# Kernel optimization log

Measured on AMD Instinct MI355X. Metric: run time of the kernel, lower is better.

Reference implementation:

```python
import jax, jax.numpy as jnp
import numpy as np

N, E = 50000, 800000
IN_DIM, E_DIM, OUT_DIM, H = 128, 32, 16, 4
NEG_SLOPE = 0.2


def setup_inputs() -> dict:
    key = jax.random.key(0)
    ks = jax.random.split(key, 9)
    return {
        "feat": jax.random.normal(ks[0], (N, IN_DIM), jnp.float32),
        "edge_attr": jax.random.normal(ks[1], (E, E_DIM), jnp.float32),
        "src": jax.random.randint(ks[2], (E,), 0, N),
        "dst": jax.random.randint(ks[3], (E,), 0, N),
        "W_fc": jax.random.normal(ks[4], (OUT_DIM * H, IN_DIM), jnp.float32) * 0.1,
        "W_edge": jax.random.normal(ks[5], (OUT_DIM * H, E_DIM), jnp.float32) * 0.1,
        "attn_h": jax.random.normal(ks[6], (1, H, OUT_DIM), jnp.float32) * 0.1,
        "attn_t": jax.random.normal(ks[7], (1, H, OUT_DIM), jnp.float32) * 0.1,
        "attn_e": jax.random.normal(ks[8], (1, H, OUT_DIM), jnp.float32) * 0.1,
        "bias": jnp.zeros((1, H, OUT_DIM), jnp.float32),
    }


def reference(feat, edge_attr, src, dst, W_fc, W_edge, attn_h, attn_t, attn_e, bias):
    n = feat.shape[0]
    # node / edge projections
    feat_ = (feat @ W_fc.T).reshape(n, H, OUT_DIM)          # [N,H,D]
    eh = (feat_ * attn_h).sum(-1)                            # [N,H]
    et = (feat_ * attn_t).sum(-1)                            # [N,H]
    feat_e = (edge_attr @ W_edge.T).reshape(-1, H, OUT_DIM)  # [E,H,D]
    ee = (feat_e * attn_e).sum(-1)                           # [E,H]
    # per-edge attention logits: u_add_e then e_add_v, then leaky relu
    e = eh[src] + ee + et[dst]                               # [E,H]
    e = jnp.where(e > 0, e, NEG_SLOPE * e)
    # edge softmax grouped by destination node
    e_max = jax.ops.segment_max(e, dst, num_segments=n)      # [N,H]
    e_max = jnp.where(jnp.isfinite(e_max), e_max, 0.0)
    a = jnp.exp(e - e_max[dst])                              # [E,H]
    a_sum = jax.ops.segment_sum(a, dst, num_segments=n)      # [N,H]
    a = a / jnp.where(a_sum[dst] > 0, a_sum[dst], 1.0)
    # u_mul_e + sum aggregation
    msg = feat_[src] * a[:, :, None]                         # [E,H,D]
    rst = jax.ops.segment_sum(msg, dst, num_segments=n)      # [N,H,D]
    rst = rst + bias
    return rst.reshape(n, H * OUT_DIM)                       # concat_out
```

## Files before the change

### kernel.cpp

```cpp
#include <hip/hip_runtime.h>

#define NN 50000
#define EE 800000
#define IND 128
#define EDD 32
#define ODD 16
#define NH 4
#define HD 64
#define NEG_SLOPE 0.2f
#define NBLK ((NN + 255) / 256)

__global__ __launch_bounds__(256)
void k_init_prep(int* __restrict__ deg, const float* __restrict__ W_fc,
                 const float* __restrict__ W_edge, const float* __restrict__ attn_e,
                 float* __restrict__ Wt, float* __restrict__ w_ee) {
    int i = blockIdx.x * 256 + threadIdx.x;
    if (i < NN) deg[i] = 0;
    if (i < HD * IND) {
        int k = i >> 6, j = i & 63;
        Wt[i] = W_fc[j * IND + k];
    }
    if (i < NH * EDD) {
        int h = i >> 5, k = i & 31;
        float s = 0.f;
        for (int d = 0; d < ODD; ++d)
            s += W_edge[(h * ODD + d) * EDD + k] * attn_e[h * ODD + d];
        w_ee[i] = s;
    }
}

__global__ __launch_bounds__(256)
void k_node(const float* __restrict__ feat, const float* __restrict__ Wt,
            const float* __restrict__ attn_h, const float* __restrict__ attn_t,
            float* __restrict__ feat_ws, float2* __restrict__ eh2,
            float2* __restrict__ et2) {
    int n = blockIdx.x * 256 + threadIdx.x;
    int half = blockIdx.y;
    if (n >= NN) return;
    const int jbase = half * 32;
    float4 row[32];
    const float4* fr4 = (const float4*)(feat + (long)n * IND);
#pragma unroll
    for (int q = 0; q < 32; ++q) row[q] = fr4[q];
    asm volatile("" ::: "memory");
    float acc[32];
#pragma unroll
    for (int j = 0; j < 32; ++j) acc[j] = 0.f;
#pragma unroll
    for (int k0 = 0; k0 < 32; ++k0) {
        float f[4] = {row[k0].x, row[k0].y, row[k0].z, row[k0].w};
#pragma unroll
        for (int kk = 0; kk < 4; ++kk) {
            const float* w = Wt + (k0 * 4 + kk) * HD + jbase;
#pragma unroll
            for (int j = 0; j < 32; ++j) acc[j] += f[kk] * w[j];
        }
    }
    float4* d4 = (float4*)(feat_ws + (long)n * HD + jbase);
#pragma unroll
    for (int q = 0; q < 8; ++q)
        d4[q] = make_float4(acc[q*4], acc[q*4+1], acc[q*4+2], acc[q*4+3]);
    float sh[2], st[2];
#pragma unroll
    for (int hh = 0; hh < 2; ++hh) {
        sh[hh] = 0.f; st[hh] = 0.f;
        int hg = half * 2 + hh;
#pragma unroll
        for (int d = 0; d < ODD; ++d) {
            float av = acc[hh * ODD + d];
            sh[hh] += av * attn_h[hg * ODD + d];
            st[hh] += av * attn_t[hg * ODD + d];
        }
    }
    eh2[n * 2 + half] = make_float2(sh[0], sh[1]);
    et2[n * 2 + half] = make_float2(st[0], st[1]);
}

__global__ __launch_bounds__(256)
void k_hist(const int* __restrict__ dst, int* __restrict__ deg, int* __restrict__ rank) {
    int e = blockIdx.x * 256 + threadIdx.x;
    if (e < EE) rank[e] = atomicAdd(&deg[dst[e]], 1);
}

__global__ __launch_bounds__(256)
void k_scan1(const int* __restrict__ deg, int* __restrict__ offs, int* __restrict__ part) {
    __shared__ int s[256];
    int t = threadIdx.x, i = blockIdx.x * 256 + t;
    int v = (i < NN) ? deg[i] : 0;
    s[t] = v;
    __syncthreads();
#pragma unroll
    for (int o = 1; o < 256; o <<= 1) {
        int u = (t >= o) ? s[t - o] : 0;
        __syncthreads();
        if (t >= o) s[t] += u;
        __syncthreads();
    }
    if (i < NN) offs[i] = s[t] - v;
    if (t == 255) part[blockIdx.x] = s[255];
}

__global__ __launch_bounds__(256)
void k_scan2(int* __restrict__ part) {
    __shared__ int s[256];
    int t = threadIdx.x;
    int v = (t < NBLK) ? part[t] : 0;
    s[t] = v;
    __syncthreads();
#pragma unroll
    for (int o = 1; o < 256; o <<= 1) {
        int u = (t >= o) ? s[t - o] : 0;
        __syncthreads();
        if (t >= o) s[t] += u;
        __syncthreads();
    }
    if (t < NBLK) part[t] = s[t] - v;
}

__global__ __launch_bounds__(256)
void k_scan3(int* __restrict__ offs, const int* __restrict__ part) {
    int i = blockIdx.x * 256 + threadIdx.x;
    if (i < NN) offs[i] += part[i >> 8];
}

__global__ __launch_bounds__(256)
void k_logit2(const float* __restrict__ edge_attr, const int* __restrict__ dst,
              const float* __restrict__ w_ee, const int* __restrict__ offs,
              const int* __restrict__ rank, float4* __restrict__ ee4,
              int* __restrict__ perm) {
    int t = blockIdx.x * 256 + threadIdx.x;
    int e0 = t * 2;
    if (e0 >= EE) return;
    int2 d2 = *(const int2*)(dst + e0);
    int2 r2 = *(const int2*)(rank + e0);
    int   o0 = offs[d2.x], o1 = offs[d2.y];
    const float4* ea = (const float4*)(edge_attr + (long)e0 * EDD);
    float4 r[16];
#pragma unroll
    for (int c = 0; c < 16; ++c) r[c] = ea[c];
    asm volatile("" ::: "memory");
    const float* f0 = (const float*)&r[0];
    const float* f1 = (const float*)&r[8];
    float x0[NH], x1[NH];
#pragma unroll
    for (int h = 0; h < NH; ++h) {
        float a = 0.f, b = 0.f;
#pragma unroll
        for (int k = 0; k < EDD; ++k) {
            float w = w_ee[h * EDD + k];
            a += f0[k] * w;
            b += f1[k] * w;
        }
        x0[h] = a; x1[h] = b;
    }
    ee4[e0]     = make_float4(x0[0], x0[1], x0[2], x0[3]);
    ee4[e0 + 1] = make_float4(x1[0], x1[1], x1[2], x1[3]);
    perm[o0 + r2.x] = e0;
    perm[o1 + r2.y] = e0 + 1;
}

__global__ __launch_bounds__(256)
void k_reduce(const int* __restrict__ offs, const int* __restrict__ deg,
              const float* __restrict__ ee, const float* __restrict__ eh,
              const float* __restrict__ et, const int* __restrict__ perm,
              const int* __restrict__ src, const float* __restrict__ feat_ws,
              const float* __restrict__ bias, float* __restrict__ out) {
    int wid = (blockIdx.x * 256 + threadIdx.x) >> 6;
    int lane = threadIdx.x & 63;
    if (wid >= NN) return;
    int start = __builtin_amdgcn_readfirstlane(offs[wid]);
    int dn    = __builtin_amdgcn_readfirstlane(deg[wid]);
    int h = lane >> 4;
    int q = lane & 15;
    float et_h = et[(long)wid * 4 + h];
    float acc = 0.f, l = 0.f;

    for (int c0 = 0; c0 < dn; c0 += 16) {
        int rem = dn - c0; if (rem > 16) rem = 16;
        int qq = (q < rem) ? q : (rem - 1);
        int   e_q = perm[start + c0 + qq];
        int   s_q = src[e_q];
        float ee_q = ee[(long)e_q * 4 + h];
        float eh_q = eh[(long)s_q * 4 + h];
        float x = ee_q + eh_q + et_h;
        x = x > 0.f ? x : NEG_SLOPE * x;
        float a_q = (q < rem) ? __expf(x) : 0.f;
        float f[16];
#pragma unroll
        for (int i = 0; i < 16; ++i) {
            int si = __shfl(s_q, i);
            f[i] = feat_ws[(long)si * HD + lane];
        }
#pragma unroll
        for (int i = 0; i < 16; ++i) {
            float ai = __shfl(a_q, (lane & 48) + i);
            l += ai;
            acc += ai * f[i];
        }
    }
    float res = (l > 0.f) ? acc / l : 0.f;
    out[(long)wid * HD + lane] = res + bias[lane];
}

extern "C" void kernel_launch(void* const* d_in, const int* in_sizes, int n_in,
                              void* d_out, int out_size, void* d_ws, size_t ws_size,
                              hipStream_t stream) {
    const float* feat      = (const float*)d_in[0];
    const float* edge_attr = (const float*)d_in[1];
    const int*   src       = (const int*)d_in[2];
    const int*   dst       = (const int*)d_in[3];
    const float* W_fc      = (const float*)d_in[4];
    const float* W_edge    = (const float*)d_in[5];
    const float* attn_h    = (const float*)d_in[6];
    const float* attn_t    = (const float*)d_in[7];
    const float* attn_e    = (const float*)d_in[8];
    const float* bias      = (const float*)d_in[9];
    float* out             = (float*)d_out;

    float* ws        = (float*)d_ws;
    float4* ee4      = (float4*)ws;
    float4* eh4      = ee4 + EE;
    float4* et4      = eh4 + NN;
    float*  feat_ws  = (float*)(et4 + NN);
    float*  Wt       = feat_ws + (long)NN * HD;
    float*  w_ee     = Wt + HD * IND;
    int*    perm     = (int*)(w_ee + NH * EDD);
    int*    rank     = perm + EE;
    int*    deg      = rank + EE;
    int*    offs     = deg + NN;
    int*    part     = offs + NN;

    k_init_prep<<<NBLK, 256, 0, stream>>>(deg, W_fc, W_edge, attn_e, Wt, w_ee);
    dim3 ngrid(NBLK, 2);
    k_node<<<ngrid, 256, 0, stream>>>(feat, Wt, attn_h, attn_t, feat_ws,
                                      (float2*)eh4, (float2*)et4);
    k_hist<<<(EE + 255) / 256, 256, 0, stream>>>(dst, deg, rank);
    k_scan1<<<NBLK, 256, 0, stream>>>(deg, offs, part);
    k_scan2<<<1, 256, 0, stream>>>(part);
    k_scan3<<<NBLK, 256, 0, stream>>>(offs, part);
    k_logit2<<<(EE / 2 + 255) / 256, 256, 0, stream>>>(edge_attr, dst, w_ee, offs, rank,
                                                       ee4, perm);
    k_reduce<<<(NN * 64 + 255) / 256, 256, 0, stream>>>(offs, deg, (const float*)ee4,
                                                        (const float*)eh4, (const float*)et4,
                                                        perm, src, feat_ws, bias, out);
}
```

Measured before the change: 336.3 us.

## Fuse edge logit+exp into sorted-order edge pass, store node features in fp16

New measurement: 383.4 us. +14.0%, slower.

```diff
diff --git a/kernel.cpp b/kernel.cpp
--- a/kernel.cpp
+++ b/kernel.cpp
@@ -10,6 +10,10 @@
 #define NEG_SLOPE 0.2f
 #define NBLK ((NN + 255) / 256)
 
+typedef float  f32x4 __attribute__((ext_vector_type(4)));
+typedef int    i32x2 __attribute__((ext_vector_type(2)));
+typedef _Float16 f16x8 __attribute__((ext_vector_type(8)));
+
 __global__ __launch_bounds__(256)
 void k_init_prep(int* __restrict__ deg, const float* __restrict__ W_fc,
                  const float* __restrict__ W_edge, const float* __restrict__ attn_e,
@@ -32,23 +36,23 @@
 __global__ __launch_bounds__(256)
 void k_node(const float* __restrict__ feat, const float* __restrict__ Wt,
             const float* __restrict__ attn_h, const float* __restrict__ attn_t,
-            float* __restrict__ feat_ws, float2* __restrict__ eh2,
+            _Float16* __restrict__ feat_h, float2* __restrict__ eh2,
             float2* __restrict__ et2) {
     int n = blockIdx.x * 256 + threadIdx.x;
-    int half = blockIdx.y;
+    int hf = blockIdx.y;
     if (n >= NN) return;
-    const int jbase = half * 32;
-    float4 row[32];
-    const float4* fr4 = (const float4*)(feat + (long)n * IND);
-#pragma unroll
-    for (int q = 0; q < 32; ++q) row[q] = fr4[q];
+    const int jbase = hf * 32;
+    f32x4 row[32];
+    const f32x4* fr4 = (const f32x4*)(feat + (long)n * IND);
+#pragma unroll
+    for (int q = 0; q < 32; ++q) row[q] = __builtin_nontemporal_load(fr4 + q);
     asm volatile("" ::: "memory");
     float acc[32];
 #pragma unroll
     for (int j = 0; j < 32; ++j) acc[j] = 0.f;
 #pragma unroll
     for (int k0 = 0; k0 < 32; ++k0) {
-        float f[4] = {row[k0].x, row[k0].y, row[k0].z, row[k0].w};
+        float f[4] = {row[k0][0], row[k0][1], row[k0][2], row[k0][3]};
 #pragma unroll
         for (int kk = 0; kk < 4; ++kk) {
             const float* w = Wt + (k0 * 4 + kk) * HD + jbase;
@@ -56,15 +60,19 @@
             for (int j = 0; j < 32; ++j) acc[j] += f[kk] * w[j];
         }
     }
-    float4* d4 = (float4*)(feat_ws + (long)n * HD + jbase);
-#pragma unroll
-    for (int q = 0; q < 8; ++q)
-        d4[q] = make_float4(acc[q*4], acc[q*4+1], acc[q*4+2], acc[q*4+3]);
+    f16x8* d8 = (f16x8*)(feat_h + (long)n * HD + jbase);
+#pragma unroll
+    for (int q = 0; q < 4; ++q) {
+        f16x8 v;
+#pragma unroll
+        for (int j = 0; j < 8; ++j) v[j] = (_Float16)acc[q * 8 + j];
+        d8[q] = v;
+    }
     float sh[2], st[2];
 #pragma unroll
     for (int hh = 0; hh < 2; ++hh) {
         sh[hh] = 0.f; st[hh] = 0.f;
-        int hg = half * 2 + hh;
+        int hg = hf * 2 + hh;
 #pragma unroll
         for (int d = 0; d < ODD; ++d) {
             float av = acc[hh * ODD + d];
@@ -72,14 +80,17 @@
             st[hh] += av * attn_t[hg * ODD + d];
         }
     }
-    eh2[n * 2 + half] = make_float2(sh[0], sh[1]);
-    et2[n * 2 + half] = make_float2(st[0], st[1]);
+    eh2[n * 2 + hf] = make_float2(sh[0], sh[1]);
+    et2[n * 2 + hf] = make_float2(st[0], st[1]);
 }
 
 __global__ __launch_bounds__(256)
 void k_hist(const int* __restrict__ dst, int* __restrict__ deg, int* __restrict__ rank) {
     int e = blockIdx.x * 256 + threadIdx.x;
-    if (e < EE) rank[e] = atomicAdd(&deg[dst[e]], 1);
+    if (e < EE) {
+        int d = __builtin_nontemporal_load(dst + e);
+        rank[e] = atomicAdd(&deg[d], 1);
+    }
 }
 
 __global__ __launch_bounds__(256)
@@ -124,24 +135,30 @@
 }
 
 __global__ __launch_bounds__(256)
-void k_logit2(const float* __restrict__ edge_attr, const int* __restrict__ dst,
-              const float* __restrict__ w_ee, const int* __restrict__ offs,
-              const int* __restrict__ rank, float4* __restrict__ ee4,
-              int* __restrict__ perm) {
+void k_edge(const float* __restrict__ edge_attr, const int* __restrict__ dst,
+            const int* __restrict__ src, const float* __restrict__ w_ee,
+            const int* __restrict__ offs, const int* __restrict__ rank,
+            const float4* __restrict__ eh4, const float4* __restrict__ et4,
+            float4* __restrict__ a4, int* __restrict__ asrc) {
     int t = blockIdx.x * 256 + threadIdx.x;
     int e0 = t * 2;
     if (e0 >= EE) return;
-    int2 d2 = *(const int2*)(dst + e0);
-    int2 r2 = *(const int2*)(rank + e0);
-    int   o0 = offs[d2.x], o1 = offs[d2.y];
-    const float4* ea = (const float4*)(edge_attr + (long)e0 * EDD);
-    float4 r[16];
-#pragma unroll
-    for (int c = 0; c < 16; ++c) r[c] = ea[c];
+    i32x2 d2 = __builtin_nontemporal_load((const i32x2*)(dst + e0));
+    i32x2 r2 = __builtin_nontemporal_load((const i32x2*)(rank + e0));
+    i32x2 s2 = __builtin_nontemporal_load((const i32x2*)(src + e0));
+    int o0 = offs[d2[0]], o1 = offs[d2[1]];
+    const f32x4* ea = (const f32x4*)(edge_attr + (long)e0 * EDD);
+    f32x4 r[16];
+#pragma unroll
+    for (int c = 0; c < 16; ++c) r[c] = __builtin_nontemporal_load(ea + c);
     asm volatile("" ::: "memory");
+    float4 eh0 = eh4[s2[0]], eh1 = eh4[s2[1]];
+    float4 et0 = et4[d2[0]], et1 = et4[d2[1]];
+    float he0[4] = {eh0.x + et0.x, eh0.y + et0.y, eh0.z + et0.z, eh0.w + et0.w};
+    float he1[4] = {eh1.x + et1.x, eh1.y + et1.y, eh1.z + et1.z, eh1.w + et1.w};
     const float* f0 = (const float*)&r[0];
     const float* f1 = (const float*)&r[8];
-    float x0[NH], x1[NH];
+    float a0[NH], a1[NH];
 #pragma unroll
     for (int h = 0; h < NH; ++h) {
         float a = 0.f, b = 0.f;
@@ -151,20 +168,24 @@
             a += f0[k] * w;
             b += f1[k] * w;
         }
-        x0[h] = a; x1[h] = b;
-    }
-    ee4[e0]     = make_float4(x0[0], x0[1], x0[2], x0[3]);
-    ee4[e0 + 1] = make_float4(x1[0], x1[1], x1[2], x1[3]);
-    perm[o0 + r2.x] = e0;
-    perm[o1 + r2.y] = e0 + 1;
+        a += he0[h]; b += he1[h];
+        a = a > 0.f ? a : NEG_SLOPE * a;
+        b = b > 0.f ? b : NEG_SLOPE * b;
+        a0[h] = __expf(a);
+        a1[h] = __expf(b);
+    }
+    int p0 = o0 + r2[0], p1 = o1 + r2[1];
+    a4[p0] = make_float4(a0[0], a0[1], a0[2], a0[3]);
+    a4[p1] = make_float4(a1[0], a1[1], a1[2], a1[3]);
+    asrc[p0] = s2[0];
+    asrc[p1] = s2[1];
 }
 
 __global__ __launch_bounds__(256)
 void k_reduce(const int* __restrict__ offs, const int* __restrict__ deg,
-              const float* __restrict__ ee, const float* __restrict__ eh,
-              const float* __restrict__ et, const int* __restrict__ perm,
-              const int* __restrict__ src, const float* __restrict__ feat_ws,
-              const float* __restrict__ bias, float* __restrict__ out) {
+              const float* __restrict__ a_f, const int* __restrict__ asrc,
+              const _Float16* __restrict__ feat_h, const float* __restrict__ bias,
+              float* __restrict__ out) {
     int wid = (blockIdx.x * 256 + threadIdx.x) >> 6;
     int lane = threadIdx.x & 63;
     if (wid >= NN) return;
@@ -172,24 +193,20 @@
     int dn    = __builtin_amdgcn_readfirstlane(deg[wid]);
     int h = lane >> 4;
     int q = lane & 15;
-    float et_h = et[(long)wid * 4 + h];
     float acc = 0.f, l = 0.f;
 
     for (int c0 = 0; c0 < dn; c0 += 16) {
         int rem = dn - c0; if (rem > 16) rem = 16;
         int qq = (q < rem) ? q : (rem - 1);
-        int   e_q = perm[start + c0 + qq];
-        int   s_q = src[e_q];
-        float ee_q = ee[(long)e_q * 4 + h];
-        float eh_q = eh[(long)s_q * 4 + h];
-        float x = ee_q + eh_q + et_h;
-        x = x > 0.f ? x : NEG_SLOPE * x;
-        float a_q = (q < rem) ? __expf(x) : 0.f;
+        int pos = start + c0 + qq;
+        int   s_q = asrc[pos];
+        float a_q = a_f[(long)pos * 4 + h];
+        if (q >= rem) a_q = 0.f;
         float f[16];
 #pragma unroll
         for (int i = 0; i < 16; ++i) {
             int si = __shfl(s_q, i);
-            f[i] = feat_ws[(long)si * HD + lane];
+            f[i] = (float)feat_h[(long)si * HD + lane];
         }
 #pragma unroll
         for (int i = 0; i < 16; ++i) {
@@ -199,7 +216,7 @@
         }
     }
     float res = (l > 0.f) ? acc / l : 0.f;
-    out[(long)wid * HD + lane] = res + bias[lane];
+    __builtin_nontemporal_store(res + bias[lane], &out[(long)wid * HD + lane]);
 }
 
 extern "C" void kernel_launch(void* const* d_in, const int* in_sizes, int n_in,
@@ -218,29 +235,28 @@
     float* out             = (float*)d_out;
 
     float* ws        = (float*)d_ws;
-    float4* ee4      = (float4*)ws;
-    float4* eh4      = ee4 + EE;
+    float4* a4       = (float4*)ws;
+    float4* eh4      = a4 + EE;
     float4* et4      = eh4 + NN;
-    float*  feat_ws  = (float*)(et4 + NN);
-    float*  Wt       = feat_ws + (long)NN * HD;
+    _Float16* feat_h = (_Float16*)(et4 + NN);
+    float*  Wt       = (float*)(feat_h + (long)NN * HD);
     float*  w_ee     = Wt + HD * IND;
-    int*    perm     = (int*)(w_ee + NH * EDD);
-    int*    rank     = perm + EE;
+    int*    asrc     = (int*)(w_ee + NH * EDD);
+    int*    rank     = asrc + EE;
     int*    deg      = rank + EE;
     int*    offs     = deg + NN;
     int*    part     = offs + NN;
 
     k_init_prep<<<NBLK, 256, 0, stream>>>(deg, W_fc, W_edge, attn_e, Wt, w_ee);
     dim3 ngrid(NBLK, 2);
-    k_node<<<ngrid, 256, 0, stream>>>(feat, Wt, attn_h, attn_t, feat_ws,
+    k_node<<<ngrid, 256, 0, stream>>>(feat, Wt, attn_h, attn_t, feat_h,
                                       (float2*)eh4, (float2*)et4);
     k_hist<<<(EE + 255) / 256, 256, 0, stream>>>(dst, deg, rank);
     k_scan1<<<NBLK, 256, 0, stream>>>(deg, offs, part);
     k_scan2<<<1, 256, 0, stream>>>(part);
     k_scan3<<<NBLK, 256, 0, stream>>>(offs, part);
-    k_logit2<<<(EE / 2 + 255) / 256, 256, 0, stream>>>(edge_attr, dst, w_ee, offs, rank,
-                                                       ee4, perm);
-    k_reduce<<<(NN * 64 + 255) / 256, 256, 0, stream>>>(offs, deg, (const float*)ee4,
-                                                        (const float*)eh4, (const float*)et4,
-                                                        perm, src, feat_ws, bias, out);
-}
+    k_edge<<<(EE / 2 + 255) / 256, 256, 0, stream>>>(edge_attr, dst, src, w_ee,
+                                                     offs, rank, eh4, et4, a4, asrc);
+    k_reduce<<<(NN * 64 + 255) / 256, 256, 0, stream>>>(offs, deg, (const float*)a4,
+                                                        asrc, feat_h, bias, out);
+}
```
